# Kernel tuning notes

Measured on AMD Instinct MI355X. Metric: run time of the kernel, lower is better.

Reference implementation:

```python
import jax, jax.numpy as jnp
import numpy as np

# constants from data_utils / args in the original repo
MPP0 = 0.2              # meter_per_pixel at process resolution
PROC_SIDE = 512.0       # process_satmap_sidelength
CAM_HEIGHT = 1.65       # camera height in meters
SHIFT_LON = 20.0        # args.shift_range_lon
SHIFT_LAT = 20.0        # args.shift_range_lat
ROT_RANGE = 10.0        # args.rotation_range (degrees)
ORI_H, ORI_W = 256, 1024  # original ground image size


def _bilinear_sample(img, uv):
    """Custom grid_sample: uv are absolute pixel coords (x,y), zero padding,
    returns (sampled [B,C,A,A], in-bounds mask [B,1,A,A])."""
    B, C, IH, IW = img.shape
    A1, A2 = uv.shape[1], uv.shape[2]
    ix, iy = uv[..., 0], uv[..., 1]
    x0 = jnp.floor(ix); y0 = jnp.floor(iy)
    x1 = x0 + 1.0;      y1 = y0 + 1.0
    w00 = (x1 - ix) * (y1 - iy)
    w01 = (ix - x0) * (y1 - iy)
    w10 = (x1 - ix) * (iy - y0)
    w11 = (ix - x0) * (iy - y0)
    valid = (ix >= 0) & (ix <= IW - 1) & (iy >= 0) & (iy <= IH - 1)
    x0c = jnp.clip(x0, 0, IW - 1).astype(jnp.int32)
    x1c = jnp.clip(x1, 0, IW - 1).astype(jnp.int32)
    y0c = jnp.clip(y0, 0, IH - 1).astype(jnp.int32)
    y1c = jnp.clip(y1, 0, IH - 1).astype(jnp.int32)
    flat = img.reshape(B, C, IH * IW)

    def gather(yy, xx):
        idx = (yy * IW + xx).reshape(B, 1, A1 * A2)
        v = jnp.take_along_axis(flat, jnp.broadcast_to(idx, (B, C, A1 * A2)), axis=2)
        return v.reshape(B, C, A1, A2)

    out = (gather(y0c, x0c) * w00[:, None]
           + gather(y0c, x1c) * w01[:, None]
           + gather(y1c, x0c) * w10[:, None]
           + gather(y1c, x1c) * w11[:, None])
    out = out * valid[:, None].astype(img.dtype)
    return out, valid[:, None]


def _sat2world(A, B, predict_height=None, dtype=jnp.float32):
    """sat pixel grid -> world XYZ1 homogeneous coords [B,A,A,4]."""
    r = jnp.arange(A, dtype=dtype)
    hh, ww = jnp.meshgrid(r, r, indexing='ij')  # hh: row index, ww: col index
    c = float(A // 2)
    mpp = MPP0 * PROC_SIDE / A
    # Aff_sat2real = mpp * [[0,1],[1,0]] applied to uv_center where uv=[w,h]
    X = jnp.broadcast_to(mpp * (hh - c), (B, A, A))
    Z = jnp.broadcast_to(mpp * (ww - c), (B, A, A))
    if predict_height is None:
        Y = jnp.zeros((B, A, A), dtype)
    else:
        Y = -predict_height[:, 0]  # [B,A,A]
    ones = jnp.ones((B, A, A), dtype)
    return jnp.stack([X, Y, Z, ones], axis=-1)


def _world2grd_uv(shift_u, shift_v, heading, XYZ1, camera_k, H, W):
    """Project world points into ground-image pixel coords. Returns (uv [B,A,A,2], depth mask [B,A,A,1])."""
    B = heading.shape[0]
    su = SHIFT_LON * shift_u[:, 0]
    sv = SHIFT_LAT * shift_v[:, 0]
    h = heading[:, 0] * (ROT_RANGE / 180.0) * jnp.pi
    cos = jnp.cos(-h); sin = jnp.sin(-h)
    z = jnp.zeros_like(cos); o = jnp.ones_like(cos)
    R = jnp.stack([cos, z, -sin, z, o, z, sin, z, cos], axis=-1).reshape(B, 3, 3)
    T = jnp.stack([sv, CAM_HEIGHT * o, -su], axis=-1)[..., None]  # [B,3,1]
    K = camera_k
    K = K.at[:, 0, :].multiply(W / ORI_W).at[:, 1, :].multiply(H / ORI_H)
    P = K @ jnp.concatenate([R, T], axis=-1)  # [B,3,4]
    uv1 = jnp.einsum('bij,bhwj->bhwi', P, XYZ1)  # [B,A,A,3]
    d = jnp.maximum(uv1[..., 2:], 1e-6)
    uv = uv1[..., :2] / d
    mask = uv1[..., 2:] > 1e-6
    return uv, mask


def setup_inputs() -> dict:
    key = jax.random.key(0)
    ks = jax.random.split(key, 6)
    B, C, H, W, A = 32, 256, 32, 128, 64
    grd_f = jax.random.normal(ks[0], (B, C, H, W), dtype=jnp.float32)
    predict_height = jax.random.uniform(ks[1], (B, 1, A, A), dtype=jnp.float32) * 2.0
    shift_u = (jax.random.uniform(ks[2], (B, 1), dtype=jnp.float32) * 2.0 - 1.0)
    shift_v = (jax.random.uniform(ks[3], (B, 1), dtype=jnp.float32) * 2.0 - 1.0)
    heading = (jax.random.uniform(ks[4], (B, 1), dtype=jnp.float32) * 2.0 - 1.0)
    fx = fy = 500.0
    K = jnp.array([[fx, 0.0, ORI_W / 2.0], [0.0, fy, ORI_H / 2.0], [0.0, 0.0, 1.0]], dtype=jnp.float32)
    camera_k = jnp.broadcast_to(K, (B, 3, 3)).copy()
    sat_embedding = jax.random.uniform(ks[5], (1, C, A, A), dtype=jnp.float32)
    return {"grd_f": grd_f, "predict_height": predict_height, "shift_u": shift_u,
            "shift_v": shift_v, "heading": heading, "camera_k": camera_k,
            "sat_embedding": sat_embedding}


def reference(grd_f, predict_height, shift_u, shift_v, heading, camera_k, sat_embedding):
    B, C, H, W = grd_f.shape
    A = sat_embedding.shape[-1]
    # project_sat_original: flat-ground (Y=0) projection
    XYZ_flat = _sat2world(A, B, None, grd_f.dtype)
    uv0, mask1 = _world2grd_uv(shift_u, shift_v, heading, XYZ_flat, camera_k, H, W)
    grd_orig, mask2 = _bilinear_sample(grd_f, uv0)
    # project_grd_to_map: height-aware projection
    XYZ_h = _sat2world(A, B, predict_height, grd_f.dtype)
    uv_h, _ = _world2grd_uv(shift_u, shift_v, heading, XYZ_h, camera_k, H, W)
    grd_h, _ = _bilinear_sample(grd_f, uv_h)
    # learned gate blend (as in inverse_map)
    out = grd_h * sat_embedding + grd_orig * (1.0 - sat_embedding)
    return out
```

## Files before the change

### kernel.cpp

```cpp
#include <hip/hip_runtime.h>
#include <math.h>

namespace {
constexpr int B_ = 32, C_ = 256, H_ = 32, W_ = 128, A_ = 64;
constexpr int AA = A_ * A_;
constexpr int HW = H_ * W_;
constexpr int CPB = 16;
constexpr int TPB = 1024;
constexpr float MPP = 1.6f;
constexpr float PI_F = 3.14159265358979323846f;
typedef float vf4 __attribute__((ext_vector_type(4)));
}

struct Pmat {
    float p00, p01, p02, p03;
    float p10, p11, p12, p13;
    float p20, p21, p22, p23;
};

__device__ __forceinline__ Pmat make_P(int b,
                                       const float* __restrict__ shift_u,
                                       const float* __restrict__ shift_v,
                                       const float* __restrict__ heading,
                                       const float* __restrict__ camk) {
    float su = 20.f * shift_u[b];
    float sv = 20.f * shift_v[b];
    float h  = heading[b] * (10.f / 180.f) * PI_F;
    float ch = cosf(h);
    float sh = -sinf(h);

    const float* K = camk + b * 9;
    float k00 = K[0] * 0.125f, k01 = K[1] * 0.125f, k02 = K[2] * 0.125f;
    float k10 = K[3] * 0.125f, k11 = K[4] * 0.125f, k12 = K[5] * 0.125f;
    float k20 = K[6],          k21 = K[7],          k22 = K[8];

    Pmat P;
    P.p00 = k00 * ch + k02 * sh;  P.p01 = k01;
    P.p02 = -k00 * sh + k02 * ch; P.p03 = k00 * sv + k01 * 1.65f - k02 * su;
    P.p10 = k10 * ch + k12 * sh;  P.p11 = k11;
    P.p12 = -k10 * sh + k12 * ch; P.p13 = k10 * sv + k11 * 1.65f - k12 * su;
    P.p20 = k20 * ch + k22 * sh;  P.p21 = k21;
    P.p22 = -k20 * sh + k22 * ch; P.p23 = k20 * sv + k21 * 1.65f - k22 * su;
    return P;
}

__device__ __forceinline__ float4 uv_at(const Pmat& P, int pos, float Y) {
    int i = pos >> 6, j = pos & 63;
    float X = MPP * (float)(i - 32);
    float Z = MPP * (float)(j - 32);

    float u1 = P.p00 * X + P.p02 * Z + P.p03;
    float v1 = P.p10 * X + P.p12 * Z + P.p13;
    float w1 = P.p20 * X + P.p22 * Z + P.p23;

    float d0 = fmaxf(w1, 1e-6f);
    float u0 = u1 / d0, v0 = v1 / d0;

    float u1h = u1 + P.p01 * Y;
    float v1h = v1 + P.p11 * Y;
    float w1h = w1 + P.p21 * Y;
    float dh = fmaxf(w1h, 1e-6f);
    float uh = u1h / dh, vh = v1h / dh;

    return make_float4(u0, v0, uh, vh);
}

__device__ __forceinline__ void mk(float ix, float iy, float4& w, int& ad) {
    bool valid = (ix >= 0.f) && (ix <= (float)(W_ - 1)) &&
                 (iy >= 0.f) && (iy <= (float)(H_ - 1));
    float x0f = floorf(ix), y0f = floorf(iy);
    float fx = ix - x0f, fy = iy - y0f;
    float xa = fminf(fmaxf(x0f, 0.f), 127.f);
    float ya = fminf(fmaxf(y0f, 0.f), 31.f);
    int a = (int)fmaf(ya, 128.f, xa);
    float gx = 1.f - fx, gy = 1.f - fy;
    w = valid ? make_float4(gx * gy, fx * gy, gx * fy, fx * fy)
              : make_float4(0.f, 0.f, 0.f, 0.f);
    ad = valid ? a : 0;
}

__device__ __forceinline__ float tap4(const float* __restrict__ im, int ad, float4 w) {
    const float* t = im + ad;
    return fmaf(w.x, t[0], fmaf(w.y, t[1], fmaf(w.z, t[128], w.w * t[129])));
}

__global__ __launch_bounds__(TPB) void proj_kernel(
        const float* __restrict__ grd,
        const float* __restrict__ sat,
        float* __restrict__ out,
        const float* __restrict__ ph,
        const float* __restrict__ shift_u,
        const float* __restrict__ shift_v,
        const float* __restrict__ heading,
        const float* __restrict__ camk) {
    __shared__ float img[2 * HW + 132];
    int cg = blockIdx.x, b = blockIdx.y;
    int c0 = cg * CPB;
    int tid = threadIdx.x;
    int p0 = tid * 4;
    int bbase = b << 12;

    const float* gbase = grd + ((size_t)b * C_ + c0) * HW;

    float4 streg = ((const float4*)gbase)[tid];

    if (tid < 33) {
        ((float4*)(img + HW))[tid] = make_float4(0.f, 0.f, 0.f, 0.f);
        ((float4*)(img + 2 * HW))[tid] = make_float4(0.f, 0.f, 0.f, 0.f);
    }

    float4 w[4][2];
    int ad[4][2];
    {
        Pmat P = make_P(b, shift_u, shift_v, heading, camk);
        const float* phb = ph + bbase;
#pragma unroll
        for (int k = 0; k < 4; ++k) {
            float4 q = uv_at(P, p0 + k, -phb[p0 + k]);
            mk(q.x, q.y, w[k][0], ad[k][0]);
            mk(q.z, q.w, w[k][1], ad[k][1]);
        }
    }

    float* outbase = out + ((size_t)b * C_ + c0) * AA + p0;
    const float* satbase = sat + (size_t)c0 * AA + p0;

#pragma unroll
    for (int cp = 0; cp < CPB; ++cp) {
        int bufo = (cp & 1) * HW;
        *(float4*)(img + bufo + p0) = streg;
        float4 nxt;
        if (cp + 1 < CPB)
            nxt = ((const float4*)(gbase + (size_t)(cp + 1) * HW))[tid];
        float4 sv = *(const float4*)(satbase + (size_t)cp * AA);
        asm volatile("s_waitcnt lgkmcnt(0)" ::: "memory");
        __builtin_amdgcn_s_barrier();

        const float* im = img + bufo;
        float r[4];
#pragma unroll
        for (int k = 0; k < 4; ++k) {
            float g0 = tap4(im, ad[k][0], w[k][0]);
            float gh = tap4(im, ad[k][1], w[k][1]);
            float s = (k == 0) ? sv.x : (k == 1) ? sv.y : (k == 2) ? sv.z : sv.w;
            r[k] = fmaf(s, gh - g0, g0);
        }
        vf4 rv = {r[0], r[1], r[2], r[3]};
        __builtin_nontemporal_store(rv, (vf4*)(outbase + (size_t)cp * AA));
        streg = nxt;
    }
}

extern "C" void kernel_launch(void* const* d_in, const int* in_sizes, int n_in,
                              void* d_out, int out_size, void* d_ws, size_t ws_size,
                              hipStream_t stream) {
    (void)in_sizes; (void)n_in; (void)out_size; (void)d_ws; (void)ws_size;
    const float* grd  = (const float*)d_in[0];
    const float* ph   = (const float*)d_in[1];
    const float* s_u  = (const float*)d_in[2];
    const float* s_v  = (const float*)d_in[3];
    const float* hd   = (const float*)d_in[4];
    const float* ck   = (const float*)d_in[5];
    const float* sat  = (const float*)d_in[6];
    float* out = (float*)d_out;

    proj_kernel<<<dim3(C_ / CPB, B_), TPB, 0, stream>>>(
        grd, sat, out, ph, s_u, s_v, hd, ck);
}
```

Baseline: 47.41 us.

## Process two channels per barrier with doubled shared-memory staging

```diff
diff --git a/kernel.cpp b/kernel.cpp
--- a/kernel.cpp
+++ b/kernel.cpp
@@ -93,7 +93,7 @@
         const float* __restrict__ shift_v,
         const float* __restrict__ heading,
         const float* __restrict__ camk) {
-    __shared__ float img[2 * HW + 132];
+    __shared__ float img[4 * HW + 132];
     int cg = blockIdx.x, b = blockIdx.y;
     int c0 = cg * CPB;
     int tid = threadIdx.x;
@@ -101,13 +101,16 @@
     int bbase = b << 12;
 
     const float* gbase = grd + ((size_t)b * C_ + c0) * HW;
+    const float* satbase = sat + (size_t)c0 * AA + p0;
+    float* outbase = out + ((size_t)b * C_ + c0) * AA + p0;
 
-    float4 streg = ((const float4*)gbase)[tid];
+    float4 imA = ((const float4*)gbase)[tid];
+    float4 imB = ((const float4*)(gbase + HW))[tid];
+    float4 svA = *(const float4*)(satbase);
+    float4 svB = *(const float4*)(satbase + (size_t)AA);
 
-    if (tid < 33) {
-        ((float4*)(img + HW))[tid] = make_float4(0.f, 0.f, 0.f, 0.f);
-        ((float4*)(img + 2 * HW))[tid] = make_float4(0.f, 0.f, 0.f, 0.f);
-    }
+    if (tid < 33)
+        ((float4*)(img + 4 * HW))[tid] = make_float4(0.f, 0.f, 0.f, 0.f);
 
     float4 w[4][2];
     int ad[4][2];
@@ -122,32 +125,42 @@
         }
     }
 
-    float* outbase = out + ((size_t)b * C_ + c0) * AA + p0;
-    const float* satbase = sat + (size_t)c0 * AA + p0;
+#pragma unroll
+    for (int pr = 0; pr < CPB / 2; ++pr) {
+        const int base = (pr & 1) * 2 * HW;
+        const int ch = pr * 2;
+        *(float4*)(img + base + p0) = imA;
+        *(float4*)(img + base + HW + p0) = imB;
 
-#pragma unroll
-    for (int cp = 0; cp < CPB; ++cp) {
-        int bufo = (cp & 1) * HW;
-        *(float4*)(img + bufo + p0) = streg;
-        float4 nxt;
-        if (cp + 1 < CPB)
-            nxt = ((const float4*)(gbase + (size_t)(cp + 1) * HW))[tid];
-        float4 sv = *(const float4*)(satbase + (size_t)cp * AA);
+        float4 nimA, nimB, nsvA, nsvB;
+        if (ch + 2 < CPB) {
+            nimA = ((const float4*)(gbase + (size_t)(ch + 2) * HW))[tid];
+            nimB = ((const float4*)(gbase + (size_t)(ch + 3) * HW))[tid];
+            nsvA = *(const float4*)(satbase + (size_t)(ch + 2) * AA);
+            nsvB = *(const float4*)(satbase + (size_t)(ch + 3) * AA);
+        }
+
         asm volatile("s_waitcnt lgkmcnt(0)" ::: "memory");
         __builtin_amdgcn_s_barrier();
 
-        const float* im = img + bufo;
-        float r[4];
 #pragma unroll
-        for (int k = 0; k < 4; ++k) {
-            float g0 = tap4(im, ad[k][0], w[k][0]);
-            float gh = tap4(im, ad[k][1], w[k][1]);
-            float s = (k == 0) ? sv.x : (k == 1) ? sv.y : (k == 2) ? sv.z : sv.w;
-            r[k] = fmaf(s, gh - g0, g0);
+        for (int half = 0; half < 2; ++half) {
+            const float* im = img + base + half * HW;
+            float4 sv = half ? svB : svA;
+            float r[4];
+#pragma unroll
+            for (int k = 0; k < 4; ++k) {
+                float g0 = tap4(im, ad[k][0], w[k][0]);
+                float gh = tap4(im, ad[k][1], w[k][1]);
+                float s = (k == 0) ? sv.x : (k == 1) ? sv.y
+                        : (k == 2) ? sv.z : sv.w;
+                r[k] = fmaf(s, gh - g0, g0);
+            }
+            vf4 rv = {r[0], r[1], r[2], r[3]};
+            __builtin_nontemporal_store(
+                rv, (vf4*)(outbase + (size_t)(ch + half) * AA));
         }
-        vf4 rv = {r[0], r[1], r[2], r[3]};
-        __builtin_nontemporal_store(rv, (vf4*)(outbase + (size_t)cp * AA));
-        streg = nxt;
+        imA = nimA; imB = nimB; svA = nsvA; svB = nsvB;
     }
 }
 
```

Result: slower. 53.78 us (+13.5%).

## Stream ground channels into LDS via direct global-to-LDS loads with deeper prefetch

Applied to the files above, without the earlier changes.

```diff
diff --git a/kernel.cpp b/kernel.cpp
--- a/kernel.cpp
+++ b/kernel.cpp
@@ -11,6 +11,8 @@
 constexpr float PI_F = 3.14159265358979323846f;
 typedef float vf4 __attribute__((ext_vector_type(4)));
 }
+
+#define SB() __builtin_amdgcn_sched_barrier(0)
 
 struct Pmat {
     float p00, p01, p02, p03;
@@ -84,6 +86,20 @@
     return fmaf(w.x, t[0], fmaf(w.y, t[1], fmaf(w.z, t[128], w.w * t[129])));
 }
 
+__device__ __forceinline__ void gll16(const float* g, float* l) {
+    __builtin_amdgcn_global_load_lds(
+        (const __attribute__((address_space(1))) void*)g,
+        (__attribute__((address_space(3))) void*)l, 16, 0, 0);
+}
+
+__device__ __forceinline__ void vmwait(int n) {
+    if (n == 6)      asm volatile("s_waitcnt vmcnt(6)" ::: "memory");
+    else if (n == 5) asm volatile("s_waitcnt vmcnt(5)" ::: "memory");
+    else if (n == 4) asm volatile("s_waitcnt vmcnt(4)" ::: "memory");
+    else if (n == 2) asm volatile("s_waitcnt vmcnt(2)" ::: "memory");
+    else             asm volatile("s_waitcnt vmcnt(0)" ::: "memory");
+}
+
 __global__ __launch_bounds__(TPB) void proj_kernel(
         const float* __restrict__ grd,
         const float* __restrict__ sat,
@@ -93,21 +109,17 @@
         const float* __restrict__ shift_v,
         const float* __restrict__ heading,
         const float* __restrict__ camk) {
-    __shared__ float img[2 * HW + 132];
+    __shared__ float img[4 * HW + 132];
     int cg = blockIdx.x, b = blockIdx.y;
     int c0 = cg * CPB;
     int tid = threadIdx.x;
     int p0 = tid * 4;
     int bbase = b << 12;
+    const int wb = (tid >> 6) << 8;
 
     const float* gbase = grd + ((size_t)b * C_ + c0) * HW;
-
-    float4 streg = ((const float4*)gbase)[tid];
-
-    if (tid < 33) {
-        ((float4*)(img + HW))[tid] = make_float4(0.f, 0.f, 0.f, 0.f);
-        ((float4*)(img + 2 * HW))[tid] = make_float4(0.f, 0.f, 0.f, 0.f);
-    }
+    const float* satbase = sat + (size_t)c0 * AA + p0;
+    float* outbase = out + ((size_t)b * C_ + c0) * AA + p0;
 
     float4 w[4][2];
     int ad[4][2];
@@ -122,32 +134,48 @@
         }
     }
 
-    float* outbase = out + ((size_t)b * C_ + c0) * AA + p0;
-    const float* satbase = sat + (size_t)c0 * AA + p0;
+    if (tid < 132) {
+        int r = tid / 33, o = (tid % 33) * 4;
+        *(float4*)(img + (r + 1) * HW + o) = make_float4(0.f, 0.f, 0.f, 0.f);
+    }
+    asm volatile("s_waitcnt lgkmcnt(0)" ::: "memory");
+    __builtin_amdgcn_s_barrier();
+
+    float4 svq[3];
+
+    SB();
+    gll16(gbase + (size_t)0 * HW + p0, img + 0 * HW + wb);
+    svq[0] = *(const float4*)(satbase);
+    gll16(gbase + (size_t)1 * HW + p0, img + 1 * HW + wb);
+    svq[1] = *(const float4*)(satbase + (size_t)AA);
+    SB();
 
 #pragma unroll
-    for (int cp = 0; cp < CPB; ++cp) {
-        int bufo = (cp & 1) * HW;
-        *(float4*)(img + bufo + p0) = streg;
-        float4 nxt;
-        if (cp + 1 < CPB)
-            nxt = ((const float4*)(gbase + (size_t)(cp + 1) * HW))[tid];
-        float4 sv = *(const float4*)(satbase + (size_t)cp * AA);
-        asm volatile("s_waitcnt lgkmcnt(0)" ::: "memory");
+    for (int k = 0; k < CPB; ++k) {
+        if (k + 2 < CPB) {
+            gll16(gbase + (size_t)(k + 2) * HW + p0,
+                  img + ((k + 2) & 3) * HW + wb);
+            svq[(k + 2) % 3] = *(const float4*)(satbase + (size_t)(k + 2) * AA);
+        }
+        SB();
+        vmwait(k == 0 ? 2 : k == 1 ? 5 : k <= 13 ? 6 : k == 14 ? 4 : 2);
         __builtin_amdgcn_s_barrier();
+        SB();
 
-        const float* im = img + bufo;
+        const float* im = img + (k & 3) * HW;
+        float4 sv = svq[k % 3];
         float r[4];
 #pragma unroll
-        for (int k = 0; k < 4; ++k) {
-            float g0 = tap4(im, ad[k][0], w[k][0]);
-            float gh = tap4(im, ad[k][1], w[k][1]);
-            float s = (k == 0) ? sv.x : (k == 1) ? sv.y : (k == 2) ? sv.z : sv.w;
-            r[k] = fmaf(s, gh - g0, g0);
+        for (int kk = 0; kk < 4; ++kk) {
+            float g0 = tap4(im, ad[kk][0], w[kk][0]);
+            float gh = tap4(im, ad[kk][1], w[kk][1]);
+            float s = (kk == 0) ? sv.x : (kk == 1) ? sv.y
+                    : (kk == 2) ? sv.z : sv.w;
+            r[kk] = fmaf(s, gh - g0, g0);
         }
         vf4 rv = {r[0], r[1], r[2], r[3]};
-        __builtin_nontemporal_store(rv, (vf4*)(outbase + (size_t)cp * AA));
-        streg = nxt;
+        __builtin_nontemporal_store(rv, (vf4*)(outbase + (size_t)k * AA));
+        SB();
     }
 }
 
```

Result: slower. 51.66 us (+9.0%).
